# Optimization experiments

Measured on AMD Instinct MI355X. Metric: run time of the kernel, lower is better.

The kernel has to match this reference:

```python
import jax, jax.numpy as jnp
import numpy as np
import math

NUM_HEAD = 16
HEAD_DIM = 64  # hidden_dim 1024 / 16 heads


def setup_inputs() -> dict:
    key = jax.random.key(0)
    ks = jax.random.split(key, 7)
    N, D = 4096, 1024
    s = 1.0 / math.sqrt(D)
    return {
        "node_emb": jax.random.normal(ks[0], (N, D), jnp.float32),
        "Wq": jax.random.normal(ks[1], (D, D), jnp.float32) * s,
        "bq": jax.random.normal(ks[2], (D,), jnp.float32) * 0.01,
        "Wk": jax.random.normal(ks[3], (D, D), jnp.float32) * s,
        "bk": jax.random.normal(ks[4], (D,), jnp.float32) * 0.01,
        "Wv": jax.random.normal(ks[5], (D, D), jnp.float32) * s,
        "bv": jax.random.normal(ks[6], (D,), jnp.float32) * 0.01,
    }


def reference(node_emb, Wq, bq, Wk, bk, Wv, bv):
    N = node_emb.shape[0]
    # QKV projections (Linear: x @ W^T-style; here W stored [in, out])
    q = (node_emb @ Wq + bq).reshape(N, NUM_HEAD, HEAD_DIM)
    k = (node_emb @ Wk + bk).reshape(N, NUM_HEAD, HEAD_DIM)
    v = (node_emb @ Wv + bv).reshape(N, NUM_HEAD, HEAD_DIM)
    # scores: [h, n_query, n_key]
    scale = 1.0 / math.sqrt(HEAD_DIM)
    scores = jnp.einsum("nhd,mhd->hnm", q, k) * scale
    attn = jax.nn.softmax(scores, axis=-1)
    out = jnp.einsum("hnm,mhd->nhd", attn, v)  # [n, h, d]
    return out.reshape(N, NUM_HEAD * HEAD_DIM)
```

## Files before the change

kernel.cpp:

```cpp
#include <hip/hip_runtime.h>
#include <hip/hip_bf16.h>

#define N_NODES 4096
#define DMODEL  1024
#define NHEAD   16
#define HDIM    64
#define NOUT    3072

typedef __attribute__((ext_vector_type(8))) short short8v;
typedef __attribute__((ext_vector_type(4))) float f32x4;
typedef __attribute__((ext_vector_type(16))) float f32x16;
typedef __attribute__((ext_vector_type(4))) unsigned short ushort4v;
typedef __attribute__((ext_vector_type(4))) unsigned int u32x4;

static __device__ __forceinline__ void gload_lds16(const void* g, void* l) {
  __builtin_amdgcn_global_load_lds((const __attribute__((address_space(1))) void*)g,
                                   (__attribute__((address_space(3))) void*)l, 16, 0, 0);
}

static __device__ __forceinline__ unsigned cvtpk(float a, float b) {
  unsigned r;
  asm("v_cvt_pk_bf16_f32 %0, %1, %2" : "=v"(r) : "v"(a), "v"(b));
  return r;
}

__global__ void prep_kernel(const float* __restrict__ x, __hip_bfloat16* __restrict__ xb,
                            const float* __restrict__ Wq, const float* __restrict__ Wk,
                            const float* __restrict__ Wv, __hip_bfloat16* __restrict__ WT) {
  __shared__ float tile[32][33];
  const int bid = blockIdx.x;
  const int t = threadIdx.x;
  if (bid < 4096) {
    int i = bid * 256 + t;
    float4 v = ((const float4*)x)[i];
    union { ushort4v u; __hip_bfloat16 h[4]; } o;
    o.h[0] = __float2bfloat16(v.x);
    o.h[1] = __float2bfloat16(v.y);
    o.h[2] = __float2bfloat16(v.z);
    o.h[3] = __float2bfloat16(v.w);
    ((ushort4v*)xb)[i] = o.u;
  } else {
    int b2 = bid - 4096;
    int z = b2 >> 10, rem = b2 & 1023;
    int bx = rem & 31, by = rem >> 5;
    const float* W = z == 0 ? Wq : (z == 1 ? Wk : Wv);
    int o0 = bx * 32, i0 = by * 32;
    int tx = t & 7, ty = t >> 3;
    {
      float4 v = *(const float4*)&W[(size_t)(i0 + ty) * DMODEL + o0 + tx * 4];
      tile[ty][tx * 4 + 0] = v.x;
      tile[ty][tx * 4 + 1] = v.y;
      tile[ty][tx * 4 + 2] = v.z;
      tile[ty][tx * 4 + 3] = v.w;
    }
    __syncthreads();
    __hip_bfloat16* outp = WT + (size_t)z * DMODEL * DMODEL;
    union { ushort4v u; __hip_bfloat16 h[4]; } o;
#pragma unroll
    for (int c = 0; c < 4; ++c) o.h[c] = __float2bfloat16(tile[tx * 4 + c][ty]);
    *(ushort4v*)&outp[(size_t)(o0 + ty) * DMODEL + i0 + tx * 4] = o.u;
  }
}

__global__ __launch_bounds__(256, 2) void gemm_qkv_kernel(
    const __hip_bfloat16* __restrict__ X, const __hip_bfloat16* __restrict__ WT,
    const float* __restrict__ bq, const float* __restrict__ bk, const float* __restrict__ bv,
    __hip_bfloat16* __restrict__ Qo, __hip_bfloat16* __restrict__ Ko, __hip_bfloat16* __restrict__ Vt) {
  __shared__ __hip_bfloat16 As[2][128 * 32];
  __shared__ __hip_bfloat16 Bs[2][128 * 32];
  const int t = threadIdx.x;
  const int lane = t & 63;
  const int w = t >> 6, wr = w >> 1, wc = w & 1;
  const int bm = blockIdx.y, bn = blockIdx.x;

  f32x4 acc[4][4] = {};

  const int rowA = t >> 2;
  const int koff = (t & 3) * 8;
  const __hip_bfloat16* Ag0 = X + (size_t)(bm * 128 + rowA) * DMODEL + koff;
  const __hip_bfloat16* Ag1 = X + (size_t)(bm * 128 + 64 + rowA) * DMODEL + koff;
  const __hip_bfloat16* Bg0 = WT + (size_t)(bn * 128 + rowA) * DMODEL + koff;
  const __hip_bfloat16* Bg1 = WT + (size_t)(bn * 128 + 64 + rowA) * DMODEL + koff;

  auto stage = [&](int kt, int b) {
    gload_lds16(Ag0 + kt * 32, &As[b][t * 8]);
    gload_lds16(Ag1 + kt * 32, &As[b][(t + 256) * 8]);
    gload_lds16(Bg0 + kt * 32, &Bs[b][t * 8]);
    gload_lds16(Bg1 + kt * 32, &Bs[b][(t + 256) * 8]);
  };

  const int fr = lane & 15, fk = (lane >> 4) * 8;

  stage(0, 0);

  for (int kt = 0; kt < DMODEL / 32; ++kt) {
    const int cur = kt & 1;
    __builtin_amdgcn_s_barrier();
    if (kt + 1 < DMODEL / 32) {
      stage(kt + 1, cur ^ 1);
      asm volatile("s_waitcnt vmcnt(4)" ::: "memory");
    } else {
      asm volatile("s_waitcnt vmcnt(0)" ::: "memory");
    }
    __builtin_amdgcn_s_barrier();
    __builtin_amdgcn_sched_barrier(0);

    const short* As_s = (const short*)As[cur];
    const short* Bs_s = (const short*)Bs[cur];
    short8v a[4], b[4];
#pragma unroll
    for (int m = 0; m < 4; ++m)
      a[m] = *(const short8v*)&As_s[(wr * 64 + m * 16 + fr) * 32 + fk];
#pragma unroll
    for (int n = 0; n < 4; ++n)
      b[n] = *(const short8v*)&Bs_s[(wc * 64 + n * 16 + fr) * 32 + fk];
#pragma unroll
    for (int m = 0; m < 4; ++m)
#pragma unroll
      for (int n = 0; n < 4; ++n)
        acc[m][n] = __builtin_amdgcn_mfma_f32_16x16x32_bf16(a[m], b[n], acc[m][n], 0, 0, 0);
  }

  const int row0 = bm * 128 + wr * 64;
  const int col0 = bn * 128 + wc * 64;
  const int which = col0 >> 10;
  const float* bias = which == 0 ? bq : (which == 1 ? bk : bv);
  const float QSCALE = 0.18033688011112042f;
#pragma unroll
  for (int m = 0; m < 4; ++m) {
#pragma unroll
    for (int n = 0; n < 4; ++n) {
#pragma unroll
      for (int i = 0; i < 4; ++i) {
        int r = row0 + m * 16 + (lane >> 4) * 4 + i;
        int c = col0 + n * 16 + (lane & 15);
        int oo = c & 1023;
        float v = acc[m][n][i] + bias[oo];
        if (which == 0) v *= QSCALE;
        int h = oo >> 6, d = oo & 63;
        __hip_bfloat16 hv = __float2bfloat16(v);
        if (which == 0)      Qo[((size_t)h << 18) + r * 64 + d] = hv;
        else if (which == 1) Ko[((size_t)h << 18) + r * 64 + d] = hv;
        else                 Vt[((size_t)h << 18) + d * 4096 + r] = hv;
      }
    }
  }
}

__global__ __launch_bounds__(256, 2) void attn64_kernel(
    const __hip_bfloat16* __restrict__ Q, const __hip_bfloat16* __restrict__ K,
    const __hip_bfloat16* __restrict__ Vt,
    __hip_bfloat16* __restrict__ Opart, float* __restrict__ lpart) {
  __shared__ __align__(16) short lds_k[2][2][64 * 64];
  __shared__ __align__(16) short lds_v[2][2][64 * 64];

  const int bid = blockIdx.x;
  const int lin = (bid & 7) * 64 + (bid >> 3);
  const int h = lin >> 5, qb = (lin & 31) >> 1, split = lin & 1;

  const int t = threadIdx.x, lane = t & 63, w = t >> 6;
  const int lq = lane & 31, hi = lane >> 5;

  const short* Qh = (const short*)Q + ((size_t)h << 18);
  const short* Kh = (const short*)K + ((size_t)h << 18);
  const short* Vh = (const short*)Vt + ((size_t)h << 18);

  const int q0 = qb * 256 + w * 64;

  short8v qfA[4], qfB[4];
#pragma unroll
  for (int kk = 0; kk < 4; ++kk) {
    qfA[kk] = *(const short8v*)&Qh[(q0 + lq) * 64 + kk * 16 + hi * 8];
    qfB[kk] = *(const short8v*)&Qh[(q0 + 32 + lq) * 64 + kk * 16 + hi * 8];
  }

  int off8[2][4];
#pragma unroll
  for (int half = 0; half < 2; ++half)
#pragma unroll
    for (int kk = 0; kk < 4; ++kk)
      off8[half][kk] = (half * 32 + lq) * 64 + (((kk * 2 + hi) ^ (lq & 7)) * 8);

  auto stage = [&](int kt, int p, int s) {
#pragma unroll
    for (int i = 0; i < 2; ++i) {
      int c = w * 128 + i * 64 + lane;
      int row = c >> 3, ss = (c & 7) ^ (row & 7);
      gload_lds16(Kh + (size_t)(kt * 64 + row) * 64 + ss * 8, &lds_k[p][s][c * 8]);
    }
#pragma unroll
    for (int i = 0; i < 2; ++i) {
      int c = w * 128 + i * 64 + lane;
      int row = c >> 3, ss = (c & 7) ^ (row & 7);
      gload_lds16(Vh + (size_t)row * 4096 + kt * 64 + ss * 8, &lds_v[p][s][c * 8]);
    }
  };

  f32x16 oA0 = {}, oA1 = {}, oB0 = {}, oB1 = {};
  float lA_r = 0.f, lB_r = 0.f;

  auto compute = [&](const short* kp, const short* vp) {
    f32x16 sA0 = {}, sA1 = {}, sB0 = {}, sB1 = {};
#pragma unroll
    for (int kk = 0; kk < 4; ++kk) {
      short8v ka0 = *(const short8v*)&kp[off8[0][kk]];
      sA0 = __builtin_amdgcn_mfma_f32_32x32x16_bf16(ka0, qfA[kk], sA0, 0, 0, 0);
      sB0 = __builtin_amdgcn_mfma_f32_32x32x16_bf16(ka0, qfB[kk], sB0, 0, 0, 0);
      short8v ka1 = *(const short8v*)&kp[off8[1][kk]];
      sA1 = __builtin_amdgcn_mfma_f32_32x32x16_bf16(ka1, qfA[kk], sA1, 0, 0, 0);
      sB1 = __builtin_amdgcn_mfma_f32_32x32x16_bf16(ka1, qfB[kk], sB1, 0, 0, 0);
    }
    short8v paA[4], paB[4];
#pragma unroll
    for (int j = 0; j < 16; ++j) { sA0[j] = __builtin_amdgcn_exp2f(sA0[j]); lA_r += sA0[j]; }
#pragma unroll
    for (int j = 0; j < 16; ++j) { sA1[j] = __builtin_amdgcn_exp2f(sA1[j]); lA_r += sA1[j]; }
#pragma unroll
    for (int half = 0; half < 2; ++half) {
      const f32x16& s = half ? sA1 : sA0;
#pragma unroll
      for (int g = 0; g < 2; ++g) {
        unsigned a0 = cvtpk(s[g * 8 + 0], s[g * 8 + 1]), a1 = cvtpk(s[g * 8 + 2], s[g * 8 + 3]);
        unsigned b0 = cvtpk(s[g * 8 + 4], s[g * 8 + 5]), b1 = cvtpk(s[g * 8 + 6], s[g * 8 + 7]);
        asm volatile("v_permlane32_swap_b32 %0, %1" : "+v"(a0), "+v"(b0));
        asm volatile("v_permlane32_swap_b32 %0, %1" : "+v"(a1), "+v"(b1));
        u32x4 u = {a0, a1, b0, b1};
        paA[half * 2 + g] = __builtin_bit_cast(short8v, u);
      }
    }
#pragma unroll
    for (int j = 0; j < 16; ++j) { sB0[j] = __builtin_amdgcn_exp2f(sB0[j]); lB_r += sB0[j]; }
#pragma unroll
    for (int j = 0; j < 16; ++j) { sB1[j] = __builtin_amdgcn_exp2f(sB1[j]); lB_r += sB1[j]; }
#pragma unroll
    for (int half = 0; half < 2; ++half) {
      const f32x16& s = half ? sB1 : sB0;
#pragma unroll
      for (int g = 0; g < 2; ++g) {
        unsigned a0 = cvtpk(s[g * 8 + 0], s[g * 8 + 1]), a1 = cvtpk(s[g * 8 + 2], s[g * 8 + 3]);
        unsigned b0 = cvtpk(s[g * 8 + 4], s[g * 8 + 5]), b1 = cvtpk(s[g * 8 + 6], s[g * 8 + 7]);
        asm volatile("v_permlane32_swap_b32 %0, %1" : "+v"(a0), "+v"(b0));
        asm volatile("v_permlane32_swap_b32 %0, %1" : "+v"(a1), "+v"(b1));
        u32x4 u = {a0, a1, b0, b1};
        paB[half * 2 + g] = __builtin_bit_cast(short8v, u);
      }
    }
#pragma unroll
    for (int kk = 0; kk < 4; ++kk) {
      short8v vb0 = *(const short8v*)&vp[off8[0][kk]];
      oA0 = __builtin_amdgcn_mfma_f32_32x32x16_bf16(paA[kk], vb0, oA0, 0, 0, 0);
      oB0 = __builtin_amdgcn_mfma_f32_32x32x16_bf16(paB[kk], vb0, oB0, 0, 0, 0);
      short8v vb1 = *(const short8v*)&vp[off8[1][kk]];
      oA1 = __builtin_amdgcn_mfma_f32_32x32x16_bf16(paA[kk], vb1, oA1, 0, 0, 0);
      oB1 = __builtin_amdgcn_mfma_f32_32x32x16_bf16(paB[kk], vb1, oB1, 0, 0, 0);
    }
  };

  const int NT = 32;
  const int NIV = NT / 2;
  const int kt0 = split * NT;

  stage(kt0 + 0, 0, 0);
  stage(kt0 + 1, 0, 1);

  for (int iv = 0; iv < NIV; ++iv) {
    const int p = iv & 1;
    __builtin_amdgcn_s_barrier();
    if (iv + 1 < NIV) {
      stage(kt0 + 2 * iv + 2, p ^ 1, 0);
      stage(kt0 + 2 * iv + 3, p ^ 1, 1);
      asm volatile("s_waitcnt vmcnt(8)" ::: "memory");
    } else {
      asm volatile("s_waitcnt vmcnt(0)" ::: "memory");
    }
    __builtin_amdgcn_s_barrier();
    __builtin_amdgcn_sched_barrier(0);
    compute(lds_k[p][0], lds_v[p][0]);
    compute(lds_k[p][1], lds_v[p][1]);
  }

  {
    float lA = lA_r + __shfl_xor(lA_r, 32);
    float lB = lB_r + __shfl_xor(lB_r, 32);
    if (hi == 0) {
      lpart[((split * NHEAD + h) << 12) + q0 + lq] = lA;
      lpart[((split * NHEAD + h) << 12) + q0 + 32 + lq] = lB;
    }
    __hip_bfloat16* Op = Opart + (size_t)split * N_NODES * DMODEL;
#pragma unroll
    for (int r = 0; r < 16; ++r) {
      int ql = (r & 3) + 8 * (r >> 2) + 4 * hi;
      int qgA = q0 + ql, qgB = q0 + 32 + ql;
      Op[(size_t)qgA * DMODEL + (h << 6) + lq] = __float2bfloat16(oA0[r]);
      Op[(size_t)qgA * DMODEL + (h << 6) + 32 + lq] = __float2bfloat16(oA1[r]);
      Op[(size_t)qgB * DMODEL + (h << 6) + lq] = __float2bfloat16(oB0[r]);
      Op[(size_t)qgB * DMODEL + (h << 6) + 32 + lq] = __float2bfloat16(oB1[r]);
    }
  }
}

__global__ void combine_kernel(const __hip_bfloat16* __restrict__ Opart,
                               const float* __restrict__ lpart,
                               float* __restrict__ out) {
  int idx = blockIdx.x * 256 + threadIdx.x;
  int n = idx >> 8;
  int c4 = idx & 255;
  int h = c4 >> 4;
  float l0 = lpart[(h << 12) + n];
  float l1 = lpart[(NHEAD << 12) + (h << 12) + n];
  float inv = 1.0f / (l0 + l1);
  ushort4v a = ((const ushort4v*)Opart)[idx];
  ushort4v b = ((const ushort4v*)(Opart + (size_t)N_NODES * DMODEL))[idx];
  f32x4 o;
#pragma unroll
  for (int j = 0; j < 4; ++j) {
    float fa = __uint_as_float((unsigned)(unsigned short)a[j] << 16);
    float fb = __uint_as_float((unsigned)(unsigned short)b[j] << 16);
    o[j] = (fa + fb) * inv;
  }
  ((f32x4*)out)[idx] = o;
}

__global__ __launch_bounds__(256, 2) void attn_single_kernel(
    const __hip_bfloat16* __restrict__ Q, const __hip_bfloat16* __restrict__ K,
    const __hip_bfloat16* __restrict__ Vt, float* __restrict__ out) {
  __shared__ __align__(16) short lds_k[2][64 * 64];
  __shared__ __align__(16) short lds_v[2][64 * 64];
  __shared__ float smc[4][32];
  const int bid = blockIdx.x;
  const int lin = (bid & 7) * 64 + (bid >> 3);
  const int h = lin >> 5, qb = lin & 31;
  const int t = threadIdx.x, lane = t & 63, w = t >> 6;
  const int lq = lane & 31, hi = lane >> 5;
  const short* Qh = (const short*)Q + ((size_t)h << 18);
  const short* Kh = (const short*)K + ((size_t)h << 18);
  const short* Vh = (const short*)Vt + ((size_t)h << 18);
  const int q0 = qb * 128 + w * 32;
  short8v qf[4];
#pragma unroll
  for (int kk = 0; kk < 4; ++kk)
    qf[kk] = *(const short8v*)&Qh[(q0 + lq) * 64 + kk * 16 + hi * 8];
  int off8[2][4];
#pragma unroll
  for (int half = 0; half < 2; ++half)
#pragma unroll
    for (int kk = 0; kk < 4; ++kk)
      off8[half][kk] = (half * 32 + lq) * 64 + (((kk * 2 + hi) ^ (lq & 7)) * 8);
  auto stage = [&](int kt, int b) {
#pragma unroll
    for (int i = 0; i < 2; ++i) {
      int c = w * 128 + i * 64 + lane;
      int row = c >> 3, ss = (c & 7) ^ (row & 7);
      gload_lds16(Kh + (size_t)(kt * 64 + row) * 64 + ss * 8, &lds_k[b][c * 8]);
    }
#pragma unroll
    for (int i = 0; i < 2; ++i) {
      int c = w * 128 + i * 64 + lane;
      int row = c >> 3, ss = (c & 7) ^ (row & 7);
      gload_lds16(Vh + (size_t)row * 4096 + kt * 64 + ss * 8, &lds_v[b][c * 8]);
    }
  };
  f32x16 o0 = {}, o1 = {};
  float l_r = 0.f;
  stage(0, 0);
  for (int kt = 0; kt < 64; ++kt) {
    const int cur = kt & 1;
    __builtin_amdgcn_s_barrier();
    if (kt + 1 < 64) {
      stage(kt + 1, cur ^ 1);
      asm volatile("s_waitcnt vmcnt(4)" ::: "memory");
    } else {
      asm volatile("s_waitcnt vmcnt(0)" ::: "memory");
    }
    __builtin_amdgcn_s_barrier();
    __builtin_amdgcn_sched_barrier(0);
    const short* kp = lds_k[cur];
    const short* vp = lds_v[cur];
    f32x16 s0 = {}, s1 = {};
#pragma unroll
    for (int kk = 0; kk < 4; ++kk) {
      short8v ka0 = *(const short8v*)&kp[off8[0][kk]];
      s0 = __builtin_amdgcn_mfma_f32_32x32x16_bf16(ka0, qf[kk], s0, 0, 0, 0);
      short8v ka1 = *(const short8v*)&kp[off8[1][kk]];
      s1 = __builtin_amdgcn_mfma_f32_32x32x16_bf16(ka1, qf[kk], s1, 0, 0, 0);
    }
#pragma unroll
    for (int j = 0; j < 16; ++j) { s0[j] = __builtin_amdgcn_exp2f(s0[j]); l_r += s0[j]; }
#pragma unroll
    for (int j = 0; j < 16; ++j) { s1[j] = __builtin_amdgcn_exp2f(s1[j]); l_r += s1[j]; }
    short8v pa[4];
#pragma unroll
    for (int half = 0; half < 2; ++half) {
      const f32x16& s = half ? s1 : s0;
#pragma unroll
      for (int g = 0; g < 2; ++g) {
        unsigned a0 = cvtpk(s[g * 8 + 0], s[g * 8 + 1]), a1 = cvtpk(s[g * 8 + 2], s[g * 8 + 3]);
        unsigned b0 = cvtpk(s[g * 8 + 4], s[g * 8 + 5]), b1 = cvtpk(s[g * 8 + 6], s[g * 8 + 7]);
        asm volatile("v_permlane32_swap_b32 %0, %1" : "+v"(a0), "+v"(b0));
        asm volatile("v_permlane32_swap_b32 %0, %1" : "+v"(a1), "+v"(b1));
        u32x4 u = {a0, a1, b0, b1};
        pa[half * 2 + g] = __builtin_bit_cast(short8v, u);
      }
    }
#pragma unroll
    for (int kk = 0; kk < 4; ++kk) {
      short8v vb0 = *(const short8v*)&vp[off8[0][kk]];
      o0 = __builtin_amdgcn_mfma_f32_32x32x16_bf16(pa[kk], vb0, o0, 0, 0, 0);
      short8v vb1 = *(const short8v*)&vp[off8[1][kk]];
      o1 = __builtin_amdgcn_mfma_f32_32x32x16_bf16(pa[kk], vb1, o1, 0, 0, 0);
    }
  }
  {
    float lt = l_r + __shfl_xor(l_r, 32);
    float inv = 1.0f / lt;
    if (lane < 32) smc[w][lq] = inv;
#pragma unroll
    for (int r = 0; r < 16; ++r) {
      int ql = (r & 3) + 8 * (r >> 2) + 4 * hi;
      float iv = smc[w][ql];
      int qg = q0 + ql;
      out[(size_t)qg * DMODEL + (h << 6) + lq] = o0[r] * iv;
      out[(size_t)qg * DMODEL + (h << 6) + 32 + lq] = o1[r] * iv;
    }
  }
}

extern "C" void kernel_launch(void* const* d_in, const int* in_sizes, int n_in,
                              void* d_out, int out_size, void* d_ws, size_t ws_size,
                              hipStream_t stream) {
  const float* node_emb = (const float*)d_in[0];
  const float* Wq = (const float*)d_in[1];
  const float* bq = (const float*)d_in[2];
  const float* Wk = (const float*)d_in[3];
  const float* bk = (const float*)d_in[4];
  const float* Wv = (const float*)d_in[5];
  const float* bv = (const float*)d_in[6];
  float* out = (float*)d_out;

  const size_t HSZ = (size_t)NHEAD * N_NODES * HDIM;
  __hip_bfloat16* Qb  = (__hip_bfloat16*)d_ws;
  __hip_bfloat16* Kb  = Qb + HSZ;
  __hip_bfloat16* Vtb = Kb + HSZ;
  __hip_bfloat16* Xbf = Vtb + HSZ;
  __hip_bfloat16* WT  = Xbf + (size_t)N_NODES * DMODEL;

  __hip_bfloat16* Opart = Xbf;
  float* lpart = (float*)(Opart + 2 * (size_t)N_NODES * DMODEL);

  const size_t split_bytes =
      (3 * HSZ + 2 * (size_t)N_NODES * DMODEL) * sizeof(__hip_bfloat16) +
      2 * (size_t)NHEAD * N_NODES * sizeof(float);
  const size_t base_bytes =
      (3 * HSZ + (size_t)N_NODES * DMODEL + (size_t)NOUT * DMODEL) * sizeof(__hip_bfloat16);
  const bool can_split = ws_size >= (split_bytes > base_bytes ? split_bytes : base_bytes);

  prep_kernel<<<4096 + 3072, 256, 0, stream>>>(node_emb, Xbf, Wq, Wk, Wv, WT);
  gemm_qkv_kernel<<<dim3(NOUT / 128, N_NODES / 128), 256, 0, stream>>>(
      Xbf, WT, bq, bk, bv, Qb, Kb, Vtb);

  if (can_split) {
    attn64_kernel<<<512, 256, 0, stream>>>(Qb, Kb, Vtb, Opart, lpart);
    combine_kernel<<<(N_NODES * DMODEL) / (256 * 4), 256, 0, stream>>>(Opart, lpart, out);
  } else {
    attn_single_kernel<<<512, 256, 0, stream>>>(Qb, Kb, Vtb, out);
  }
}
```

Baseline: 131.6 us.

## Split attention KV range three ways with triple-buffered single-tile pipeline

Changes the split-K attention from two KV halves to three uneven splits (22/21/21 tiles), raising the grid from 512 to 768 blocks so more work is spread across the CUs. The LDS pipeline is restructured from double-buffered pairs of tiles to a rotating triple buffer of single tiles with one barrier per tile. The combine kernel now sums three partial outputs and normalizers, which adds extra workspace traffic and an extra partial write/read pass.

```diff
diff --git a/kernel.cpp b/kernel.cpp
--- a/kernel.cpp
+++ b/kernel.cpp
@@ -151,12 +151,17 @@
     const __hip_bfloat16* __restrict__ Q, const __hip_bfloat16* __restrict__ K,
     const __hip_bfloat16* __restrict__ Vt,
     __hip_bfloat16* __restrict__ Opart, float* __restrict__ lpart) {
-  __shared__ __align__(16) short lds_k[2][2][64 * 64];
-  __shared__ __align__(16) short lds_v[2][2][64 * 64];
+  __shared__ __align__(16) short lds_k[3 * 64 * 64];
+  __shared__ __align__(16) short lds_v[3 * 64 * 64];
 
   const int bid = blockIdx.x;
-  const int lin = (bid & 7) * 64 + (bid >> 3);
-  const int h = lin >> 5, qb = (lin & 31) >> 1, split = lin & 1;
+  const int lin = (bid & 7) * 96 + (bid >> 3);
+  const int h = lin / 48;
+  const int rem = lin % 48;
+  const int qb = rem / 3, split = rem % 3;
+
+  const int kt0 = (split == 0) ? 0 : (22 + 21 * (split - 1));
+  const int ktN = kt0 + ((split == 0) ? 22 : 21);
 
   const int t = threadIdx.x, lane = t & 63, w = t >> 6;
   const int lq = lane & 31, hi = lane >> 5;
@@ -181,18 +186,18 @@
     for (int kk = 0; kk < 4; ++kk)
       off8[half][kk] = (half * 32 + lq) * 64 + (((kk * 2 + hi) ^ (lq & 7)) * 8);
 
-  auto stage = [&](int kt, int p, int s) {
+  auto stage = [&](int kt, int boff) {
 #pragma unroll
     for (int i = 0; i < 2; ++i) {
       int c = w * 128 + i * 64 + lane;
       int row = c >> 3, ss = (c & 7) ^ (row & 7);
-      gload_lds16(Kh + (size_t)(kt * 64 + row) * 64 + ss * 8, &lds_k[p][s][c * 8]);
+      gload_lds16(Kh + (size_t)(kt * 64 + row) * 64 + ss * 8, &lds_k[boff + c * 8]);
     }
 #pragma unroll
     for (int i = 0; i < 2; ++i) {
       int c = w * 128 + i * 64 + lane;
       int row = c >> 3, ss = (c & 7) ^ (row & 7);
-      gload_lds16(Vh + (size_t)row * 4096 + kt * 64 + ss * 8, &lds_v[p][s][c * 8]);
+      gload_lds16(Vh + (size_t)row * 4096 + kt * 64 + ss * 8, &lds_v[boff + c * 8]);
     }
   };
 
@@ -256,27 +261,21 @@
     }
   };
 
-  const int NT = 32;
-  const int NIV = NT / 2;
-  const int kt0 = split * NT;
-
-  stage(kt0 + 0, 0, 0);
-  stage(kt0 + 1, 0, 1);
-
-  for (int iv = 0; iv < NIV; ++iv) {
-    const int p = iv & 1;
-    __builtin_amdgcn_s_barrier();
-    if (iv + 1 < NIV) {
-      stage(kt0 + 2 * iv + 2, p ^ 1, 0);
-      stage(kt0 + 2 * iv + 3, p ^ 1, 1);
-      asm volatile("s_waitcnt vmcnt(8)" ::: "memory");
+  stage(kt0, 0);
+  int bS = 4096, bC = 0;
+
+  for (int kt = kt0; kt < ktN; ++kt) {
+    if (kt + 1 < ktN) {
+      stage(kt + 1, bS);
+      asm volatile("s_waitcnt vmcnt(4)" ::: "memory");
     } else {
       asm volatile("s_waitcnt vmcnt(0)" ::: "memory");
     }
     __builtin_amdgcn_s_barrier();
     __builtin_amdgcn_sched_barrier(0);
-    compute(lds_k[p][0], lds_v[p][0]);
-    compute(lds_k[p][1], lds_v[p][1]);
+    compute(lds_k + bC, lds_v + bC);
+    bC = bS;
+    bS = (bS == 8192) ? 0 : (bS + 4096);
   }
 
   {
@@ -306,19 +305,19 @@
   int n = idx >> 8;
   int c4 = idx & 255;
   int h = c4 >> 4;
-  float l0 = lpart[(h << 12) + n];
-  float l1 = lpart[(NHEAD << 12) + (h << 12) + n];
-  float inv = 1.0f / (l0 + l1);
-  ushort4v a = ((const ushort4v*)Opart)[idx];
-  ushort4v b = ((const ushort4v*)(Opart + (size_t)N_NODES * DMODEL))[idx];
-  f32x4 o;
-#pragma unroll
-  for (int j = 0; j < 4; ++j) {
-    float fa = __uint_as_float((unsigned)(unsigned short)a[j] << 16);
-    float fb = __uint_as_float((unsigned)(unsigned short)b[j] << 16);
-    o[j] = (fa + fb) * inv;
-  }
-  ((f32x4*)out)[idx] = o;
+  float l = 0.f;
+#pragma unroll
+  for (int s = 0; s < 3; ++s) l += lpart[((s * NHEAD + h) << 12) + n];
+  float inv = 1.0f / l;
+  f32x4 o = {};
+#pragma unroll
+  for (int s = 0; s < 3; ++s) {
+    ushort4v a = ((const ushort4v*)(Opart + (size_t)s * N_NODES * DMODEL))[idx];
+#pragma unroll
+    for (int j = 0; j < 4; ++j)
+      o[j] += __uint_as_float((unsigned)(unsigned short)a[j] << 16);
+  }
+  ((f32x4*)out)[idx] = o * inv;
 }
 
 __global__ __launch_bounds__(256, 2) void attn_single_kernel(
@@ -445,11 +444,11 @@
   __hip_bfloat16* WT  = Xbf + (size_t)N_NODES * DMODEL;
 
   __hip_bfloat16* Opart = Xbf;
-  float* lpart = (float*)(Opart + 2 * (size_t)N_NODES * DMODEL);
+  float* lpart = (float*)(Opart + 3 * (size_t)N_NODES * DMODEL);
 
   const size_t split_bytes =
-      (3 * HSZ + 2 * (size_t)N_NODES * DMODEL) * sizeof(__hip_bfloat16) +
-      2 * (size_t)NHEAD * N_NODES * sizeof(float);
+      (3 * HSZ + 3 * (size_t)N_NODES * DMODEL) * sizeof(__hip_bfloat16) +
+      3 * (size_t)NHEAD * N_NODES * sizeof(float);
   const size_t base_bytes =
       (3 * HSZ + (size_t)N_NODES * DMODEL + (size_t)NOUT * DMODEL) * sizeof(__hip_bfloat16);
   const bool can_split = ws_size >= (split_bytes > base_bytes ? split_bytes : base_bytes);
@@ -459,7 +458,7 @@
       Xbf, WT, bq, bk, bv, Qb, Kb, Vtb);
 
   if (can_split) {
-    attn64_kernel<<<512, 256, 0, stream>>>(Qb, Kb, Vtb, Opart, lpart);
+    attn64_kernel<<<768, 256, 0, stream>>>(Qb, Kb, Vtb, Opart, lpart);
     combine_kernel<<<(N_NODES * DMODEL) / (256 * 4), 256, 0, stream>>>(Opart, lpart, out);
   } else {
     attn_single_kernel<<<512, 256, 0, stream>>>(Qb, Kb, Vtb, out);
```

New measurement: 135.0 us. 1.03x slower.
